# Kernel optimization log

Measured on AMD Instinct MI355X. Metric: run time of the kernel, lower is better.

## Reference

```python
import jax, jax.numpy as jnp
import numpy as np

TAU = 0.5

def _l2norm(x, eps=1e-12):
    n = jnp.linalg.norm(x, axis=-1, keepdims=True)
    return x / jnp.maximum(n, eps)

def _gat(a, idx):
    # per-rating gather: a [R, N, ...], idx [R, E] -> [R, E, ...]
    return jax.vmap(lambda x, j: x[j])(a, idx)

def setup_inputs() -> dict:
    key = jax.random.key(0)
    R, Nu, Nm, E, F, d, Dr, OUT = 5, 50000, 20000, 100000, 4, 16, 64, 64
    ks = jax.random.split(key, 17)
    inp = {
        "user_feat_k": jax.random.normal(ks[0], (R, Nu, d), jnp.float32),
        "movie_feat_k": jax.random.normal(ks[1], (R, Nm, d), jnp.float32),
        "user_feat_sum": 0.1 * jax.random.normal(ks[2], (R, Nu, F, d), jnp.float32),
        "movie_feat_sum": 0.1 * jax.random.normal(ks[3], (R, Nm, F, d), jnp.float32),
        "review_feat": 0.1 * jax.random.normal(ks[4], (R, E, F, Dr), jnp.float32),
        "prototypes": 0.1 * jax.random.normal(ks[5], (F, Dr), jnp.float32),
        "eta": jax.random.normal(ks[6], (R, E), jnp.float32),
        "node_w_fwd": 0.25 * jax.random.normal(ks[7], (R, d, d), jnp.float32),
        "review_w_fwd": 0.1 * jax.random.normal(ks[8], (R, d, Dr), jnp.float32),
        "node_w_rev": 0.25 * jax.random.normal(ks[9], (R, d, d), jnp.float32),
        "review_w_rev": 0.1 * jax.random.normal(ks[10], (R, d, Dr), jnp.float32),
        "ufc_w": 0.25 * jax.random.normal(ks[11], (OUT, d), jnp.float32),
        "ufc_b": jnp.zeros((OUT,), jnp.float32),
        "ifc_w": 0.25 * jax.random.normal(ks[12], (OUT, d), jnp.float32),
        "ifc_b": jnp.zeros((OUT,), jnp.float32),
        "edges_u": jax.random.randint(ks[13], (R, E), 0, Nu, jnp.int64),
        "edges_m": jax.random.randint(ks[14], (R, E), 0, Nm, jnp.int64),
        "k": 1,
    }
    return inp

def reference(user_feat_k, movie_feat_k, user_feat_sum, movie_feat_sum,
              review_feat, prototypes, eta, node_w_fwd, review_w_fwd,
              node_w_rev, review_w_rev, ufc_w, ufc_b, ifc_w, ifc_b,
              edges_u, edges_m, k):
    R, E = edges_u.shape
    Nu = user_feat_k.shape[1]
    Nm = movie_feat_k.shape[1]

    # ---- per-edge contrastive weights (vectorized over R ratings) ----
    row_feat = _l2norm(_gat(user_feat_k, edges_u))          # [R,E,d]
    col_feat = _l2norm(_gat(movie_feat_k, edges_m))         # [R,E,d]
    sim_k = (row_feat * col_feat).sum(-1) / TAU             # [R,E]
    sim_all = (_gat(user_feat_sum, edges_u) * _gat(movie_feat_sum, edges_m)).sum(-1) / TAU  # [R,E,F]
    exp_sim = jnp.exp(sim_k) / jnp.exp(sim_all).sum(-1)

    rf_k = review_feat[:, :, k, :]                          # [R,E,Dr]
    ad_k = jnp.einsum('red,d->re', rf_k, prototypes[k]) / TAU
    ad_all = jnp.einsum('refd,fd->ref', review_feat, prototypes) / TAU
    exp_anchor = jnp.exp(ad_k) / jnp.exp(ad_all).sum(-1)

    g = jax.nn.sigmoid(eta[:, :E])                          # eta[rating][:E]
    w = g * exp_anchor + (1.0 - g) * exp_sim                # [R,E]

    # ---- scatter-normalize (fwd + rev etypes give identical w, so the
    #      original's (sum over both)/2 equals a single-direction sum) ----
    norm_user = jax.ops.segment_sum(w.reshape(-1), edges_u.reshape(-1), num_segments=Nu)
    norm_movie = jax.ops.segment_sum(w.reshape(-1), edges_m.reshape(-1), num_segments=Nm)
    n_ij = jnp.sqrt(norm_user[edges_u] * norm_movie[edges_m])  # [R,E]
    w_norm = w / n_ij
    int_dist = w_norm.reshape(R * E, 1)                     # movie->user etypes, rating order

    # ---- GCMC hetero conv: gather src, add projected review feat, scale, scatter ----
    hu = jnp.einsum('rnd,rod->rno', user_feat_k, node_w_fwd)     # node_w per fwd etype
    rfp_f = jnp.einsum('red,rod->reo', rf_k, review_w_fwd)
    msg_m = (_gat(hu, edges_u) + rfp_f) * w_norm[..., None]      # [R,E,d]
    ifeat = jax.ops.segment_sum(msg_m.reshape(R * E, -1), edges_m.reshape(-1), num_segments=Nm)

    hm = jnp.einsum('rnd,rod->rno', movie_feat_k, node_w_rev)    # node_w per rev etype
    rfp_r = jnp.einsum('red,rod->reo', rf_k, review_w_rev)
    msg_u = (_gat(hm, edges_m) + rfp_r) * w_norm[..., None]
    ufeat = jax.ops.segment_sum(msg_u.reshape(R * E, -1), edges_u.reshape(-1), num_segments=Nu)

    lrelu = lambda x: jnp.where(x >= 0, x, 0.1 * x)
    ufeat = lrelu(ufeat) @ ufc_w.T + ufc_b
    ifeat = lrelu(ifeat) @ ifc_w.T + ifc_b
    return (ufeat, ifeat, int_dist)
```

## Files before the change

### kernel.cpp

```cpp
#include <hip/hip_runtime.h>

#define TAU_INV 2.0f
#define R_ 5
#define NU 50000
#define NM 20000
#define EDGES 100000
#define F_ 4
#define D_ 16
#define DR 64
#define OUT_ 64
#define EPW 16

__device__ __forceinline__ float dot4(float4 a, float4 b) {
    return a.x * b.x + a.y * b.y + a.z * b.z + a.w * b.w;
}

__global__ __launch_bounds__(256) void k_edge_w(
    const float* __restrict__ ufk, const float* __restrict__ mfk,
    const float* __restrict__ ufs, const float* __restrict__ mfs,
    const float* __restrict__ rfeat, const float* __restrict__ proto,
    const float* __restrict__ eta, const int* __restrict__ eu,
    const int* __restrict__ em, const int* __restrict__ kp,
    float* __restrict__ wbuf, float* __restrict__ nrm_u, float* __restrict__ nrm_m)
{
    const int tid = threadIdx.x;
    const int wv = tid >> 6, l = tid & 63;
    const int g16 = l >> 4;
    const int j   = l & 15;
    const int r = blockIdx.y;
    int e = (blockIdx.x * 4 + wv) * 4 + g16;
    const bool live = (e < EDGES);
    if (e >= EDGES) e = EDGES - 1;
    const int idx = r * EDGES + e;
    const int u = eu[idx], m = em[idx];
    const int kk = kp[0];

    const float4 pu = ((const float4*)(ufs + (size_t)(r * NU + u) * 64))[j];
    const float4 pm = ((const float4*)(mfs + (size_t)(r * NM + m) * 64))[j];
    float p = dot4(pu, pm);
    p += __shfl_xor(p, 1); p += __shfl_xor(p, 2);
    const float es = expf(p * TAU_INV);
    float dsim = es;
    dsim += __shfl_xor(dsim, 4); dsim += __shfl_xor(dsim, 8);

    const int jc = j & 3;
    const float4 u4 = ((const float4*)(ufk + (size_t)(r * NU + u) * 16))[jc];
    const float4 m4 = ((const float4*)(mfk + (size_t)(r * NM + m) * 16))[jc];
    float su = dot4(u4, u4), sm = dot4(m4, m4), sd = dot4(u4, m4);
    su += __shfl_xor(su, 1); su += __shfl_xor(su, 2);
    sm += __shfl_xor(sm, 1); sm += __shfl_xor(sm, 2);
    sd += __shfl_xor(sd, 1); sd += __shfl_xor(sd, 2);
    const float nsim = expf(sd / (fmaxf(sqrtf(su), 1e-12f) * fmaxf(sqrtf(sm), 1e-12f)) * TAU_INV);

    const float4* rf4 = (const float4*)(rfeat + (size_t)idx * 256);
    const float4* pr4 = (const float4*)proto;
    const int base = (j >> 2) * 16 + (j & 3) * 4;
    float ap = 0.f;
#pragma unroll
    for (int t = 0; t < 4; ++t)
        ap += dot4(rf4[base + t], pr4[base + t]);
    ap += __shfl_xor(ap, 1); ap += __shfl_xor(ap, 2);
    const float ea = expf(ap * TAU_INV);
    float dan = ea;
    dan += __shfl_xor(dan, 4); dan += __shfl_xor(dan, 8);
    const float adk = __shfl(ap, (l & 48) | (kk << 2));
    const float na = expf(adk * TAU_INV);

    const float gt = 1.0f / (1.0f + expf(-eta[idx]));
    const float w = gt * (na / dan) + (1.0f - gt) * (nsim / dsim);

    if (live && j == 0) {
        wbuf[idx] = w;
        atomicAdd(&nrm_u[u], w);
        atomicAdd(&nrm_m[m], w);
    }
}

__global__ __launch_bounds__(256) void k_edge_msg(
    const float* __restrict__ ufk, const float* __restrict__ mfk,
    const float* __restrict__ rfeat,
    const float* __restrict__ nwf, const float* __restrict__ rwf,
    const float* __restrict__ nwr, const float* __restrict__ rwr,
    const int* __restrict__ eu, const int* __restrict__ em, const int* __restrict__ kp,
    const float* __restrict__ wbuf, const float* __restrict__ nrm_u,
    const float* __restrict__ nrm_m,
    float* __restrict__ upre, float* __restrict__ ipre, float* __restrict__ dist_out)
{
    __shared__ __align__(16) float4 lds[4][EPW * 24];

    const int tid = threadIdx.x;
    const int wv = tid >> 6, l = tid & 63;
    const int o = l & 15, q = l >> 4;
    const int r = blockIdx.y;
    const int kk = kp[0];
    const int rE = r * EDGES;

    const float4* pwf = (const float4*)(rwf + (size_t)r * 1024 + o * 64 + q * 16);
    const float4* pwr = (const float4*)(rwr + (size_t)r * 1024 + o * 64 + q * 16);
    const float4 wf0 = pwf[0], wf1 = pwf[1], wf2 = pwf[2], wf3 = pwf[3];
    const float4 wr0 = pwr[0], wr1 = pwr[1], wr2 = pwr[2], wr3 = pwr[3];
    const float4 nf = *(const float4*)(nwf + r * 256 + o * 16 + q * 4);
    const float4 nr = *(const float4*)(nwr + r * 256 + o * 16 + q * 4);

    const int ebase = (blockIdx.x * 4 + wv) * EPW;

    int eu16, em16; float wn16;
    {
        int e2 = ebase + (l & 15); if (e2 >= EDGES) e2 = EDGES - 1;
        eu16 = eu[rE + e2]; em16 = em[rE + e2];
        const float w0 = wbuf[rE + e2];
        wn16 = w0 / sqrtf(nrm_u[eu16] * nrm_m[em16]);
    }

    if (l < EPW && ebase + l < EDGES)
        dist_out[rE + ebase + l] = wn16;

    float4 st[6];
#pragma unroll
    for (int t = 0; t < 6; ++t) {
        const int s = l + 64 * t;
        const int j = s / 24;
        const int p = s % 24;
        int e2 = ebase + j; if (e2 >= EDGES) e2 = EDGES - 1;
        const int uj = __shfl(eu16, j);
        const int mj = __shfl(em16, j);
        const float4* src;
        if (p < 16)      src = (const float4*)(rfeat + ((size_t)(rE + e2) * 4 + kk) * 64) + p;
        else if (p < 20) src = (const float4*)(ufk + (size_t)(r * NU + uj) * 16) + (p - 16);
        else             src = (const float4*)(mfk + (size_t)(r * NM + mj) * 16) + (p - 20);
        st[t] = *src;
    }
#pragma unroll
    for (int t = 0; t < 6; ++t)
        lds[wv][l + 64 * t] = st[t];

#pragma unroll
    for (int j = 0; j < EPW; j += 2) {
        float amv[2], auv[2];
#pragma unroll
        for (int s = 0; s < 2; ++s) {
            const float4* L = &lds[wv][(j + s) * 24];
            const float4 a0 = L[q * 4 + 0];
            const float4 a1 = L[q * 4 + 1];
            const float4 a2 = L[q * 4 + 2];
            const float4 a3 = L[q * 4 + 3];
            const float4 uf = L[16 + q];
            const float4 mf = L[20 + q];

            float am = dot4(a0, wf0) + dot4(a1, wf1) + dot4(a2, wf2) + dot4(a3, wf3)
                     + dot4(uf, nf);
            float au = dot4(a0, wr0) + dot4(a1, wr1) + dot4(a2, wr2) + dot4(a3, wr3)
                     + dot4(mf, nr);
            am += __shfl_xor(am, 16); am += __shfl_xor(am, 32);
            au += __shfl_xor(au, 16); au += __shfl_xor(au, 32);
            const float wn = __shfl(wn16, j + s);
            amv[s] = am * wn; auv[s] = au * wn;
        }

        const int u0 = __shfl(eu16, j),     m0 = __shfl(em16, j);
        const int u1 = __shfl(eu16, j + 1), m1 = __shfl(em16, j + 1);

        const int  half = l >> 5;
        const bool liveA = (ebase + j + half) < EDGES;
        float  val;
        float* base;
        if (half == 0) {
            val  = (l < 16) ? amv[0] : auv[0];
            base = (l < 16) ? &ipre[(size_t)m0 * 16 + o] : &upre[(size_t)u0 * 16 + o];
        } else {
            val  = (l < 48) ? amv[1] : auv[1];
            base = (l < 48) ? &ipre[(size_t)m1 * 16 + o] : &upre[(size_t)u1 * 16 + o];
        }
        if (liveA) atomicAdd(base, val);
    }
}

__global__ __launch_bounds__(256) void k_fc(
    const float* __restrict__ upre, const float* __restrict__ ipre,
    const float* __restrict__ uw, const float* __restrict__ ub,
    const float* __restrict__ iw, const float* __restrict__ ib,
    float* __restrict__ out_u, float* __restrict__ out_i)
{
    const int tid = threadIdx.x;
    const int n = blockIdx.x * 4 + (tid >> 6);
    if (n >= NU + NM) return;
    const int o = tid & 63;
    const float* pre; const float* W; const float* B; float* dst;
    if (n < NU) { pre = upre + (size_t)n * 16; W = uw; B = ub; dst = out_u + (size_t)n * 64; }
    else { int n2 = n - NU; pre = ipre + (size_t)n2 * 16; W = iw; B = ib; dst = out_i + (size_t)n2 * 64; }
    float acc = B[o];
#pragma unroll
    for (int d = 0; d < 16; d++) {
        float x = pre[d];
        x = x >= 0.f ? x : 0.1f * x;
        acc += x * W[o * 16 + d];
    }
    dst[o] = acc;
}

extern "C" void kernel_launch(void* const* d_in, const int* in_sizes, int n_in,
                              void* d_out, int out_size, void* d_ws, size_t ws_size,
                              hipStream_t stream) {
    const float* ufk  = (const float*)d_in[0];
    const float* mfk  = (const float*)d_in[1];
    const float* ufs  = (const float*)d_in[2];
    const float* mfs  = (const float*)d_in[3];
    const float* rfe  = (const float*)d_in[4];
    const float* pro  = (const float*)d_in[5];
    const float* eta  = (const float*)d_in[6];
    const float* nwf  = (const float*)d_in[7];
    const float* rwf  = (const float*)d_in[8];
    const float* nwr  = (const float*)d_in[9];
    const float* rwr  = (const float*)d_in[10];
    const float* uw   = (const float*)d_in[11];
    const float* ub   = (const float*)d_in[12];
    const float* iw   = (const float*)d_in[13];
    const float* ib   = (const float*)d_in[14];
    const int*   eu   = (const int*)d_in[15];
    const int*   em   = (const int*)d_in[16];
    const int*   kp   = (const int*)d_in[17];

    float* out    = (float*)d_out;
    float* out_u  = out;
    float* out_i  = out + (size_t)NU * 64;
    float* out_d  = out_i + (size_t)NM * 64;

    float* ws    = (float*)d_ws;
    float* nrm_u = ws;
    float* nrm_m = nrm_u + NU;
    float* upre  = nrm_m + NM;
    float* ipre  = upre + (size_t)NU * 16;
    float* wbuf  = ipre + (size_t)NM * 16;

    const size_t zeroN = (size_t)NU + NM + (size_t)NU * 16 + (size_t)NM * 16;
    hipMemsetAsync(d_ws, 0, zeroN * sizeof(float), stream);

    dim3 gW((EDGES + 15) / 16, R_);
    k_edge_w<<<gW, 256, 0, stream>>>(ufk, mfk, ufs, mfs, rfe, pro, eta, eu, em, kp,
                                     wbuf, nrm_u, nrm_m);
    dim3 gM((EDGES + 4 * EPW - 1) / (4 * EPW), R_);
    k_edge_msg<<<gM, 256, 0, stream>>>(ufk, mfk, rfe, nwf, rwf, nwr, rwr, eu, em, kp,
                                       wbuf, nrm_u, nrm_m, upre, ipre, out_d);
    k_fc<<<((NU + NM) + 3) / 4, 256, 0, stream>>>(upre, ipre, uw, ub, iw, ib, out_u, out_i);
}
```

Measured before the change: 252.0 us.

## Compute edge message projections with bf16 MFMA and 32 edges per wave

Replaces the per-lane fp32 dot-product projection of review, user and movie features with bf16 16x16x32 MFMA instructions. Staged features are converted to bf16 in shared memory, and the node and review weight matrices are packed into MFMA B operands. Each wave now handles 32 edges instead of 16. This trades fp32 precision for bf16 and raises register pressure, which may lower occupancy. The kernel is likely limited by gathers and atomics, so the compute savings may matter little.

```diff
diff --git a/kernel.cpp b/kernel.cpp
--- a/kernel.cpp
+++ b/kernel.cpp
@@ -1,4 +1,5 @@
 #include <hip/hip_runtime.h>
+#include <hip/hip_bf16.h>
 
 #define TAU_INV 2.0f
 #define R_ 5
@@ -9,10 +10,27 @@
 #define D_ 16
 #define DR 64
 #define OUT_ 64
-#define EPW 16
+#define EPW 32
+
+typedef __attribute__((ext_vector_type(8))) short short8;
+typedef __attribute__((ext_vector_type(4))) float f32x4;
 
 __device__ __forceinline__ float dot4(float4 a, float4 b) {
     return a.x * b.x + a.y * b.y + a.z * b.z + a.w * b.w;
+}
+
+__device__ __forceinline__ ushort f2bf(float x) {
+    __hip_bfloat16 h = __float2bfloat16(x);
+    return *reinterpret_cast<ushort*>(&h);
+}
+
+__device__ __forceinline__ short8 pack8(float4 lo, float4 hi) {
+    short8 v;
+    v[0] = (short)f2bf(lo.x); v[1] = (short)f2bf(lo.y);
+    v[2] = (short)f2bf(lo.z); v[3] = (short)f2bf(lo.w);
+    v[4] = (short)f2bf(hi.x); v[5] = (short)f2bf(hi.y);
+    v[6] = (short)f2bf(hi.z); v[7] = (short)f2bf(hi.w);
+    return v;
 }
 
 __global__ __launch_bounds__(256) void k_edge_w(
@@ -86,7 +104,7 @@
     const float* __restrict__ nrm_m,
     float* __restrict__ upre, float* __restrict__ ipre, float* __restrict__ dist_out)
 {
-    __shared__ __align__(16) float4 lds[4][EPW * 24];
+    __shared__ __align__(16) ushort s_a[4][EPW][104];
 
     const int tid = threadIdx.x;
     const int wv = tid >> 6, l = tid & 63;
@@ -95,83 +113,89 @@
     const int kk = kp[0];
     const int rE = r * EDGES;
 
-    const float4* pwf = (const float4*)(rwf + (size_t)r * 1024 + o * 64 + q * 16);
-    const float4* pwr = (const float4*)(rwr + (size_t)r * 1024 + o * 64 + q * 16);
-    const float4 wf0 = pwf[0], wf1 = pwf[1], wf2 = pwf[2], wf3 = pwf[3];
-    const float4 wr0 = pwr[0], wr1 = pwr[1], wr2 = pwr[2], wr3 = pwr[3];
-    const float4 nf = *(const float4*)(nwf + r * 256 + o * 16 + q * 4);
-    const float4 nr = *(const float4*)(nwr + r * 256 + o * 16 + q * 4);
+    short8 Bf[3], Br[3];
+    {
+        const float* wfp = rwf + (size_t)r * 1024 + o * 64;
+        const float* wrp = rwr + (size_t)r * 1024 + o * 64;
+        const float* nfp = nwf + r * 256 + o * 16;
+        const float* nrp = nwr + r * 256 + o * 16;
+#pragma unroll
+        for (int sl = 0; sl < 2; ++sl) {
+            const int bk = 32 * sl + 8 * q;
+            Bf[sl] = pack8(*(const float4*)(wfp + bk), *(const float4*)(wfp + bk + 4));
+            Br[sl] = pack8(*(const float4*)(wrp + bk), *(const float4*)(wrp + bk + 4));
+        }
+        const short8 z8 = {0, 0, 0, 0, 0, 0, 0, 0};
+        Bf[2] = (q < 2) ? pack8(*(const float4*)(nfp + 8 * q),
+                                *(const float4*)(nfp + 8 * q + 4)) : z8;
+        Br[2] = (q >= 2) ? pack8(*(const float4*)(nrp + 8 * (q - 2)),
+                                 *(const float4*)(nrp + 8 * (q - 2) + 4)) : z8;
+    }
 
     const int ebase = (blockIdx.x * 4 + wv) * EPW;
 
-    int eu16, em16; float wn16;
+    int eu32, em32; float wn32;
     {
-        int e2 = ebase + (l & 15); if (e2 >= EDGES) e2 = EDGES - 1;
-        eu16 = eu[rE + e2]; em16 = em[rE + e2];
+        int e2 = ebase + (l & 31); if (e2 >= EDGES) e2 = EDGES - 1;
+        eu32 = eu[rE + e2]; em32 = em[rE + e2];
         const float w0 = wbuf[rE + e2];
-        wn16 = w0 / sqrtf(nrm_u[eu16] * nrm_m[em16]);
-    }
-
-    if (l < EPW && ebase + l < EDGES)
-        dist_out[rE + ebase + l] = wn16;
-
-    float4 st[6];
-#pragma unroll
-    for (int t = 0; t < 6; ++t) {
+        wn32 = w0 / sqrtf(nrm_u[eu32] * nrm_m[em32]);
+    }
+    if (l < 32 && ebase + l < EDGES)
+        dist_out[rE + ebase + l] = wn32;
+
+    float4 st[12];
+#pragma unroll
+    for (int t = 0; t < 12; ++t) {
         const int s = l + 64 * t;
         const int j = s / 24;
         const int p = s % 24;
         int e2 = ebase + j; if (e2 >= EDGES) e2 = EDGES - 1;
-        const int uj = __shfl(eu16, j);
-        const int mj = __shfl(em16, j);
+        const int uj = __shfl(eu32, j);
+        const int mj = __shfl(em32, j);
         const float4* src;
         if (p < 16)      src = (const float4*)(rfeat + ((size_t)(rE + e2) * 4 + kk) * 64) + p;
         else if (p < 20) src = (const float4*)(ufk + (size_t)(r * NU + uj) * 16) + (p - 16);
         else             src = (const float4*)(mfk + (size_t)(r * NM + mj) * 16) + (p - 20);
         st[t] = *src;
     }
-#pragma unroll
-    for (int t = 0; t < 6; ++t)
-        lds[wv][l + 64 * t] = st[t];
-
-#pragma unroll
-    for (int j = 0; j < EPW; j += 2) {
-        float amv[2], auv[2];
-#pragma unroll
-        for (int s = 0; s < 2; ++s) {
-            const float4* L = &lds[wv][(j + s) * 24];
-            const float4 a0 = L[q * 4 + 0];
-            const float4 a1 = L[q * 4 + 1];
-            const float4 a2 = L[q * 4 + 2];
-            const float4 a3 = L[q * 4 + 3];
-            const float4 uf = L[16 + q];
-            const float4 mf = L[20 + q];
-
-            float am = dot4(a0, wf0) + dot4(a1, wf1) + dot4(a2, wf2) + dot4(a3, wf3)
-                     + dot4(uf, nf);
-            float au = dot4(a0, wr0) + dot4(a1, wr1) + dot4(a2, wr2) + dot4(a3, wr3)
-                     + dot4(mf, nr);
-            am += __shfl_xor(am, 16); am += __shfl_xor(am, 32);
-            au += __shfl_xor(au, 16); au += __shfl_xor(au, 32);
-            const float wn = __shfl(wn16, j + s);
-            amv[s] = am * wn; auv[s] = au * wn;
+    char* abase = (char*)&s_a[wv][0][0];
+#pragma unroll
+    for (int t = 0; t < 12; ++t) {
+        const int s = l + 64 * t;
+        const int j = s / 24;
+        const int p = s % 24;
+        uint2 wds;
+        wds.x = (uint)f2bf(st[t].x) | ((uint)f2bf(st[t].y) << 16);
+        wds.y = (uint)f2bf(st[t].z) | ((uint)f2bf(st[t].w) << 16);
+        *(uint2*)(abase + j * 208 + p * 8) = wds;
+    }
+
+#pragma unroll
+    for (int g = 0; g < 2; ++g) {
+        f32x4 accm = {0.f, 0.f, 0.f, 0.f};
+        f32x4 accu = {0.f, 0.f, 0.f, 0.f};
+        const int row = g * 16 + o;
+#pragma unroll
+        for (int sl = 0; sl < 3; ++sl) {
+            const short8 a = *(const short8*)(abase + row * 208 + (sl * 32 + 8 * q) * 2);
+            accm = __builtin_amdgcn_mfma_f32_16x16x32_bf16(a, Bf[sl], accm, 0, 0, 0);
+            accu = __builtin_amdgcn_mfma_f32_16x16x32_bf16(a, Br[sl], accu, 0, 0, 0);
         }
-
-        const int u0 = __shfl(eu16, j),     m0 = __shfl(em16, j);
-        const int u1 = __shfl(eu16, j + 1), m1 = __shfl(em16, j + 1);
-
-        const int  half = l >> 5;
-        const bool liveA = (ebase + j + half) < EDGES;
-        float  val;
-        float* base;
-        if (half == 0) {
-            val  = (l < 16) ? amv[0] : auv[0];
-            base = (l < 16) ? &ipre[(size_t)m0 * 16 + o] : &upre[(size_t)u0 * 16 + o];
-        } else {
-            val  = (l < 48) ? amv[1] : auv[1];
-            base = (l < 48) ? &ipre[(size_t)m1 * 16 + o] : &upre[(size_t)u1 * 16 + o];
+#pragma unroll
+        for (int i = 0; i < 4; ++i) {
+            const int j = g * 16 + q * 4 + i;
+            const float wnj = __shfl(wn32, j);
+            const int   uj  = __shfl(eu32, j);
+            const int   mj  = __shfl(em32, j);
+            const bool  livej = (ebase + j) < EDGES;
+            const float vm = accm[i] * wnj;
+            const float vu = accu[i] * wnj;
+            if (livej) {
+                atomicAdd(&ipre[(size_t)mj * 16 + o], vm);
+                atomicAdd(&upre[(size_t)uj * 16 + o], vu);
+            }
         }
-        if (liveA) atomicAdd(base, val);
     }
 }
 
```

After: 245.0 us (median of 2 runs). 1.03x faster.

## Fuse message projection into edge-weight kernel and store bf16 messages for scatter

Applied to the files above, without the earlier changes.

Moves the per-edge review/node projection from the message kernel into the edge-weight kernel, which already loads the same edge indices and review features, and writes unnormalized messages to a workspace as packed bf16 pairs. A new lightweight scatter kernel reads the packed messages, applies the normalized weight and does the atomic adds. This avoids re-reading the review feature slice and node features in a second pass, at the cost of an extra bf16 intermediate buffer and some lost message precision. Bounds checks are removed, which relies on EDGES being a multiple of the per-block edge count.

```diff
diff --git a/kernel.cpp b/kernel.cpp
--- a/kernel.cpp
+++ b/kernel.cpp
@@ -1,4 +1,5 @@
 #include <hip/hip_runtime.h>
+#include <hip/hip_bf16.h>
 
 #define TAU_INV 2.0f
 #define R_ 5
@@ -9,10 +10,19 @@
 #define D_ 16
 #define DR 64
 #define OUT_ 64
-#define EPW 16
 
 __device__ __forceinline__ float dot4(float4 a, float4 b) {
     return a.x * b.x + a.y * b.y + a.z * b.z + a.w * b.w;
+}
+
+__device__ __forceinline__ ushort f2bf(float x) {
+    __hip_bfloat16 h = __float2bfloat16(x);
+    return *reinterpret_cast<ushort*>(&h);
+}
+
+__device__ __forceinline__ float bf2f(ushort u) {
+    uint v = ((uint)u) << 16;
+    return *reinterpret_cast<float*>(&v);
 }
 
 __global__ __launch_bounds__(256) void k_edge_w(
@@ -21,19 +31,29 @@
     const float* __restrict__ rfeat, const float* __restrict__ proto,
     const float* __restrict__ eta, const int* __restrict__ eu,
     const int* __restrict__ em, const int* __restrict__ kp,
-    float* __restrict__ wbuf, float* __restrict__ nrm_u, float* __restrict__ nrm_m)
+    const float* __restrict__ nwf, const float* __restrict__ rwf,
+    const float* __restrict__ nwr, const float* __restrict__ rwr,
+    float* __restrict__ wbuf, float* __restrict__ nrm_u, float* __restrict__ nrm_m,
+    uint* __restrict__ msg)
 {
     const int tid = threadIdx.x;
     const int wv = tid >> 6, l = tid & 63;
     const int g16 = l >> 4;
     const int j   = l & 15;
     const int r = blockIdx.y;
-    int e = (blockIdx.x * 4 + wv) * 4 + g16;
-    const bool live = (e < EDGES);
-    if (e >= EDGES) e = EDGES - 1;
-    const int idx = r * EDGES + e;
+    const int rE = r * EDGES;
+    const int e = (blockIdx.x * 4 + wv) * 4 + g16;
+    const int idx = rE + e;
     const int u = eu[idx], m = em[idx];
     const int kk = kp[0];
+
+    const int o = j, q = g16;
+    const float4* pwf = (const float4*)(rwf + (size_t)r * 1024 + o * 64 + q * 16);
+    const float4* pwr = (const float4*)(rwr + (size_t)r * 1024 + o * 64 + q * 16);
+    const float4 wfA = pwf[0], wfB = pwf[1], wfC = pwf[2], wfD = pwf[3];
+    const float4 wrA = pwr[0], wrB = pwr[1], wrC = pwr[2], wrD = pwr[3];
+    const float4 nf = *(const float4*)(nwf + r * 256 + o * 16 + q * 4);
+    const float4 nr = *(const float4*)(nwr + r * 256 + o * 16 + q * 4);
 
     const float4 pu = ((const float4*)(ufs + (size_t)(r * NU + u) * 64))[j];
     const float4 pm = ((const float4*)(mfs + (size_t)(r * NM + m) * 64))[j];
@@ -69,110 +89,74 @@
     const float gt = 1.0f / (1.0f + expf(-eta[idx]));
     const float w = gt * (na / dan) + (1.0f - gt) * (nsim / dsim);
 
-    if (live && j == 0) {
+    if (j == 0) {
         wbuf[idx] = w;
         atomicAdd(&nrm_u[u], w);
         atomicAdd(&nrm_m[m], w);
     }
-}
-
-__global__ __launch_bounds__(256) void k_edge_msg(
-    const float* __restrict__ ufk, const float* __restrict__ mfk,
-    const float* __restrict__ rfeat,
-    const float* __restrict__ nwf, const float* __restrict__ rwf,
-    const float* __restrict__ nwr, const float* __restrict__ rwr,
-    const int* __restrict__ eu, const int* __restrict__ em, const int* __restrict__ kp,
+
+    float amv[4], auv[4];
+#pragma unroll
+    for (int s = 0; s < 4; ++s) {
+        const int e_s   = (blockIdx.x * 4 + wv) * 4 + s;
+        const int idx_s = rE + e_s;
+        const int u_s = __shfl(u, s * 16);
+        const int m_s = __shfl(m, s * 16);
+
+        const float4* rk = (const float4*)(rfeat + ((size_t)idx_s * 4 + kk) * 64) + q * 4;
+        const float4 a0 = rk[0], a1 = rk[1], a2 = rk[2], a3 = rk[3];
+        const float4 uf = ((const float4*)(ufk + (size_t)(r * NU + u_s) * 16))[q];
+        const float4 mf = ((const float4*)(mfk + (size_t)(r * NM + m_s) * 16))[q];
+
+        float am = dot4(a0, wfA) + dot4(a1, wfB) + dot4(a2, wfC) + dot4(a3, wfD)
+                 + dot4(uf, nf);
+        float au = dot4(a0, wrA) + dot4(a1, wrB) + dot4(a2, wrC) + dot4(a3, wrD)
+                 + dot4(mf, nr);
+        am += __shfl_xor(am, 16); am += __shfl_xor(am, 32);
+        au += __shfl_xor(au, 16); au += __shfl_xor(au, 32);
+        amv[s] = am; auv[s] = au;
+    }
+    const uint pk = (uint)f2bf(amv[g16]) | ((uint)f2bf(auv[g16]) << 16);
+    msg[(size_t)idx * 16 + o] = pk;
+}
+
+__global__ __launch_bounds__(256) void k_scatter(
+    const int* __restrict__ eu, const int* __restrict__ em,
     const float* __restrict__ wbuf, const float* __restrict__ nrm_u,
-    const float* __restrict__ nrm_m,
+    const float* __restrict__ nrm_m, const uint* __restrict__ msg,
     float* __restrict__ upre, float* __restrict__ ipre, float* __restrict__ dist_out)
 {
-    __shared__ __align__(16) float4 lds[4][EPW * 24];
-
     const int tid = threadIdx.x;
     const int wv = tid >> 6, l = tid & 63;
-    const int o = l & 15, q = l >> 4;
+    const int o = l & 15;
     const int r = blockIdx.y;
-    const int kk = kp[0];
     const int rE = r * EDGES;
-
-    const float4* pwf = (const float4*)(rwf + (size_t)r * 1024 + o * 64 + q * 16);
-    const float4* pwr = (const float4*)(rwr + (size_t)r * 1024 + o * 64 + q * 16);
-    const float4 wf0 = pwf[0], wf1 = pwf[1], wf2 = pwf[2], wf3 = pwf[3];
-    const float4 wr0 = pwr[0], wr1 = pwr[1], wr2 = pwr[2], wr3 = pwr[3];
-    const float4 nf = *(const float4*)(nwf + r * 256 + o * 16 + q * 4);
-    const float4 nr = *(const float4*)(nwr + r * 256 + o * 16 + q * 4);
-
-    const int ebase = (blockIdx.x * 4 + wv) * EPW;
-
-    int eu16, em16; float wn16;
-    {
-        int e2 = ebase + (l & 15); if (e2 >= EDGES) e2 = EDGES - 1;
-        eu16 = eu[rE + e2]; em16 = em[rE + e2];
-        const float w0 = wbuf[rE + e2];
-        wn16 = w0 / sqrtf(nrm_u[eu16] * nrm_m[em16]);
-    }
-
-    if (l < EPW && ebase + l < EDGES)
-        dist_out[rE + ebase + l] = wn16;
-
-    float4 st[6];
-#pragma unroll
-    for (int t = 0; t < 6; ++t) {
-        const int s = l + 64 * t;
-        const int j = s / 24;
-        const int p = s % 24;
-        int e2 = ebase + j; if (e2 >= EDGES) e2 = EDGES - 1;
-        const int uj = __shfl(eu16, j);
-        const int mj = __shfl(em16, j);
-        const float4* src;
-        if (p < 16)      src = (const float4*)(rfeat + ((size_t)(rE + e2) * 4 + kk) * 64) + p;
-        else if (p < 20) src = (const float4*)(ufk + (size_t)(r * NU + uj) * 16) + (p - 16);
-        else             src = (const float4*)(mfk + (size_t)(r * NM + mj) * 16) + (p - 20);
-        st[t] = *src;
-    }
-#pragma unroll
-    for (int t = 0; t < 6; ++t)
-        lds[wv][l + 64 * t] = st[t];
-
-#pragma unroll
-    for (int j = 0; j < EPW; j += 2) {
-        float amv[2], auv[2];
-#pragma unroll
-        for (int s = 0; s < 2; ++s) {
-            const float4* L = &lds[wv][(j + s) * 24];
-            const float4 a0 = L[q * 4 + 0];
-            const float4 a1 = L[q * 4 + 1];
-            const float4 a2 = L[q * 4 + 2];
-            const float4 a3 = L[q * 4 + 3];
-            const float4 uf = L[16 + q];
-            const float4 mf = L[20 + q];
-
-            float am = dot4(a0, wf0) + dot4(a1, wf1) + dot4(a2, wf2) + dot4(a3, wf3)
-                     + dot4(uf, nf);
-            float au = dot4(a0, wr0) + dot4(a1, wr1) + dot4(a2, wr2) + dot4(a3, wr3)
-                     + dot4(mf, nr);
-            am += __shfl_xor(am, 16); am += __shfl_xor(am, 32);
-            au += __shfl_xor(au, 16); au += __shfl_xor(au, 32);
-            const float wn = __shfl(wn16, j + s);
-            amv[s] = am * wn; auv[s] = au * wn;
-        }
-
-        const int u0 = __shfl(eu16, j),     m0 = __shfl(em16, j);
-        const int u1 = __shfl(eu16, j + 1), m1 = __shfl(em16, j + 1);
+    const int ebase = (blockIdx.x * 4 + wv) * 8;
+
+    float wnsave = 0.f;
+#pragma unroll
+    for (int j = 0; j < 8; j += 2) {
+        const int e0 = ebase + j, e1 = e0 + 1;
+        const int u0 = eu[rE + e0], m0 = em[rE + e0];
+        const int u1 = eu[rE + e1], m1 = em[rE + e1];
+        const float wn0 = wbuf[rE + e0] / sqrtf(nrm_u[u0] * nrm_m[m0]);
+        const float wn1 = wbuf[rE + e1] / sqrtf(nrm_u[u1] * nrm_m[m1]);
+        if (l == j)     wnsave = wn0;
+        if (l == j + 1) wnsave = wn1;
 
         const int  half = l >> 5;
-        const bool liveA = (ebase + j + half) < EDGES;
-        float  val;
-        float* base;
-        if (half == 0) {
-            val  = (l < 16) ? amv[0] : auv[0];
-            base = (l < 16) ? &ipre[(size_t)m0 * 16 + o] : &upre[(size_t)u0 * 16 + o];
-        } else {
-            val  = (l < 48) ? amv[1] : auv[1];
-            base = (l < 48) ? &ipre[(size_t)m1 * 16 + o] : &upre[(size_t)u1 * 16 + o];
-        }
-        if (liveA) atomicAdd(base, val);
-    }
+        const int  eh   = half ? e1 : e0;
+        const uint pk   = msg[(size_t)(rE + eh) * 16 + o];
+        const float wnh = half ? wn1 : wn0;
+        const bool up   = (l & 31) >= 16;
+        const float val = bf2f(up ? (ushort)(pk >> 16) : (ushort)(pk & 0xffff)) * wnh;
+        const int  uh   = half ? u1 : u0;
+        const int  mh   = half ? m1 : m0;
+        float* basep = up ? &upre[(size_t)uh * 16 + o] : &ipre[(size_t)mh * 16 + o];
+        atomicAdd(basep, val);
+    }
+    if (l < 8)
+        dist_out[rE + ebase + l] = wnsave;
 }
 
 __global__ __launch_bounds__(256) void k_fc(
@@ -231,15 +215,16 @@
     float* upre  = nrm_m + NM;
     float* ipre  = upre + (size_t)NU * 16;
     float* wbuf  = ipre + (size_t)NM * 16;
+    uint*  msg   = (uint*)(wbuf + (size_t)R_ * EDGES);
 
     const size_t zeroN = (size_t)NU + NM + (size_t)NU * 16 + (size_t)NM * 16;
     hipMemsetAsync(d_ws, 0, zeroN * sizeof(float), stream);
 
     dim3 gW((EDGES + 15) / 16, R_);
     k_edge_w<<<gW, 256, 0, stream>>>(ufk, mfk, ufs, mfs, rfe, pro, eta, eu, em, kp,
-                                     wbuf, nrm_u, nrm_m);
-    dim3 gM((EDGES + 4 * EPW - 1) / (4 * EPW), R_);
-    k_edge_msg<<<gM, 256, 0, stream>>>(ufk, mfk, rfe, nwf, rwf, nwr, rwr, eu, em, kp,
-                                       wbuf, nrm_u, nrm_m, upre, ipre, out_d);
+                                     nwf, rwf, nwr, rwr, wbuf, nrm_u, nrm_m, msg);
+    dim3 gS(EDGES / 32, R_);
+    k_scatter<<<gS, 256, 0, stream>>>(eu, em, wbuf, nrm_u, nrm_m, msg,
+                                      upre, ipre, out_d);
     k_fc<<<((NU + NM) + 3) / 4, 256, 0, stream>>>(upre, ipre, uw, ub, iw, ib, out_u, out_i);
 }
```

After: 390.8 us. 55.1% more time.
